# Optimization experiments

Hardware: AMD Instinct MI355X
Metric: run time of the kernel (lower is better)

The kernel has to match this reference:

```python
import jax, jax.numpy as jnp
import numpy as np

B, N, H = 32, 512, 128
LN_EPS = 1e-5

def _layernorm(x):
    # LayerNorm over last dim, no affine (elementwise_affine=False)
    mu = jnp.mean(x, axis=-1, keepdims=True)
    var = jnp.var(x, axis=-1, keepdims=True)
    return (x - mu) * jax.lax.rsqrt(var + LN_EPS)

def setup_inputs() -> dict:
    key = jax.random.key(0)
    k0, k1, k2, k3 = jax.random.split(key, 4)
    s = jax.random.normal(k0, (B, N, H), dtype=jnp.float32)
    ev = jax.random.normal(k1, (B, N, N, 3), dtype=jnp.float32)
    mask = (jax.random.uniform(k2, (B, N, N, 1)) > 0.5).astype(jnp.float32)
    W1 = jax.random.normal(k3, (H, H), dtype=jnp.float32) / np.sqrt(H)
    b1 = jnp.zeros((H,), dtype=jnp.float32)
    return {"s": s, "ev": ev, "mask": mask, "W1": W1, "b1": b1}

def reference(s, ev, mask, W1, b1):
    # lin1: Linear -> LayerNorm (no affine) -> SiLU
    h = jnp.einsum('bnh,kh->bnk', s, W1) + b1          # (B, N, H)
    h = jax.nn.silu(_layernorm(h))
    # Fused CFConv: v[b,i,c,d] = sum_j mask[b,i,j] * ev[b,i,j,c] * h[b,j,d]
    mev = ev * mask                                     # (B, N, N, 3)
    v = jnp.einsum('bijc,bjd->bicd', mev, h)            # (B, N, 3, H)
    return v
```

## Files before the change

kernel.cpp:

```cpp
#include <hip/hip_runtime.h>
#include <hip/hip_bf16.h>

#define B_ 32
#define N_ 512
#define H_ 128

typedef float f32x4 __attribute__((ext_vector_type(4)));
typedef short short8 __attribute__((ext_vector_type(8)));
typedef short short4v __attribute__((ext_vector_type(4)));

static __device__ __forceinline__ float bf2f(unsigned short u) {
  union { unsigned int ui; float f; } x;
  x.ui = ((unsigned int)u) << 16;
  return x.f;
}
static __device__ __forceinline__ unsigned short f2bf(float f) {
  __hip_bfloat16 h = __float2bfloat16(f);
  return *reinterpret_cast<unsigned short*>(&h);
}

__global__ __launch_bounds__(256, 2) void lin_ln_silu_kernel(
    const float* __restrict__ s, const float* __restrict__ W1,
    const float* __restrict__ b1, unsigned short* __restrict__ h_t) {
  __shared__ unsigned short sA[32 * 136];
  __shared__ unsigned short wB[128 * 136];
  __shared__ unsigned short ht_sh[128 * 40];
  __shared__ float buf[4][32][2];
  const int t = threadIdx.x;
  const int b = blockIdx.y;
  const int n0 = blockIdx.x * 32;
  const int w = t >> 6, l = t & 63;
  const int l15 = l & 15, quad = l >> 4;

#pragma unroll
  for (int r = 0; r < 16; ++r) {
    int q = t + 256 * r;
    int d = q >> 5, part = q & 31;
    float4 v = *reinterpret_cast<const float4*>(W1 + d * H_ + part * 4);
    short4v wv;
    wv.x = (short)f2bf(v.x); wv.y = (short)f2bf(v.y);
    wv.z = (short)f2bf(v.z); wv.w = (short)f2bf(v.w);
    *reinterpret_cast<short4v*>(&wB[d * 136 + part * 4]) = wv;
  }
#pragma unroll
  for (int r = 0; r < 4; ++r) {
    int q = t + 256 * r;
    int n = q >> 5, part = q & 31;
    float4 v = *reinterpret_cast<const float4*>(
        s + ((size_t)b * N_ + n0 + n) * H_ + part * 4);
    short4v sv;
    sv.x = (short)f2bf(v.x); sv.y = (short)f2bf(v.y);
    sv.z = (short)f2bf(v.z); sv.w = (short)f2bf(v.w);
    *reinterpret_cast<short4v*>(&sA[n * 136 + part * 4]) = sv;
  }
  __syncthreads();

  f32x4 acc[2][2];
#pragma unroll
  for (int mt = 0; mt < 2; ++mt)
#pragma unroll
    for (int ct = 0; ct < 2; ++ct)
#pragma unroll
      for (int e = 0; e < 4; ++e) acc[mt][ct][e] = 0.f;

#pragma unroll
  for (int ks = 0; ks < 4; ++ks) {
    short8 av[2], bv[2];
#pragma unroll
    for (int mt = 0; mt < 2; ++mt)
      av[mt] = *reinterpret_cast<const short8*>(
          &sA[(mt * 16 + l15) * 136 + ks * 32 + quad * 8]);
#pragma unroll
    for (int ct = 0; ct < 2; ++ct)
      bv[ct] = *reinterpret_cast<const short8*>(
          &wB[(w * 32 + ct * 16 + l15) * 136 + ks * 32 + quad * 8]);
#pragma unroll
    for (int mt = 0; mt < 2; ++mt)
#pragma unroll
      for (int ct = 0; ct < 2; ++ct)
        acc[mt][ct] = __builtin_amdgcn_mfma_f32_16x16x32_bf16(
            av[mt], bv[ct], acc[mt][ct], 0, 0, 0);
  }

  const float bb[2] = {b1[w * 32 + l15], b1[w * 32 + 16 + l15]};
#pragma unroll
  for (int mt = 0; mt < 2; ++mt)
#pragma unroll
    for (int ct = 0; ct < 2; ++ct)
#pragma unroll
      for (int e = 0; e < 4; ++e) acc[mt][ct][e] += bb[ct];

  float s1[2][4], s2[2][4];
#pragma unroll
  for (int mt = 0; mt < 2; ++mt)
#pragma unroll
    for (int r = 0; r < 4; ++r) {
      float x0 = acc[mt][0][r], x1 = acc[mt][1][r];
      s1[mt][r] = x0 + x1;
      s2[mt][r] = x0 * x0 + x1 * x1;
    }
#pragma unroll
  for (int off = 1; off <= 8; off <<= 1) {
#pragma unroll
    for (int mt = 0; mt < 2; ++mt)
#pragma unroll
      for (int r = 0; r < 4; ++r) {
        s1[mt][r] += __shfl_xor(s1[mt][r], off);
        s2[mt][r] += __shfl_xor(s2[mt][r], off);
      }
  }
  if (l15 == 0) {
#pragma unroll
    for (int mt = 0; mt < 2; ++mt)
#pragma unroll
      for (int r = 0; r < 4; ++r) {
        int row = mt * 16 + quad * 4 + r;
        buf[w][row][0] = s1[mt][r];
        buf[w][row][1] = s2[mt][r];
      }
  }
  __syncthreads();

#pragma unroll
  for (int mt = 0; mt < 2; ++mt)
#pragma unroll
    for (int r = 0; r < 4; ++r) {
      int row = mt * 16 + quad * 4 + r;
      float S1 = buf[0][row][0] + buf[1][row][0] + buf[2][row][0] +
                 buf[3][row][0];
      float S2 = buf[0][row][1] + buf[1][row][1] + buf[2][row][1] +
                 buf[3][row][1];
      float mean = S1 * (1.f / 128.f);
      float var = S2 * (1.f / 128.f) - mean * mean;
      float rs = rsqrtf(var + 1e-5f);
#pragma unroll
      for (int ct = 0; ct < 2; ++ct) {
        float x = (acc[mt][ct][r] - mean) * rs;
        float y = x / (1.f + __expf(-x));
        ht_sh[(w * 32 + ct * 16 + l15) * 40 + row] = f2bf(y);
      }
    }
  __syncthreads();

#pragma unroll
  for (int r = 0; r < 2; ++r) {
    int q = t + 256 * r;
    int d = q >> 2, part = q & 3;
    float4 v = *reinterpret_cast<const float4*>(&ht_sh[d * 40 + part * 8]);
    *reinterpret_cast<float4*>(
        h_t + ((size_t)b * 128 + d) * 512 + n0 + part * 8) = v;
  }
}

__global__ __launch_bounds__(256, 1) void cfconv_mfma_kernel(
    const float* __restrict__ ev, const float* __restrict__ mask,
    const unsigned short* __restrict__ h_t, float* __restrict__ out) {
  __shared__ unsigned short hL[128 * 512];
  const int t = threadIdx.x;
  const int b = blockIdx.y;
  const int i0 = blockIdx.x * 64;
  const int w = t >> 6, l = t & 63;
  const int l15 = l & 15, quad = l >> 4;
  const int ig = i0 + w * 16 + l15;

  {
    const unsigned short* hb = h_t + (size_t)b * 65536;
#pragma unroll 4
    for (int r2 = 0; r2 < 32; ++r2) {
      int row = w * 32 + r2;
      float4 v = *reinterpret_cast<const float4*>(hb + row * 512 + l * 8);
      *reinterpret_cast<float4*>(
          &hL[row * 512 + (l >> 3) * 64 + (((l & 7) ^ (row & 7)) * 8)]) = v;
    }
  }
  __syncthreads();

  f32x4 acc[3][8];
#pragma unroll
  for (int mt = 0; mt < 3; ++mt)
#pragma unroll
    for (int nt = 0; nt < 8; ++nt)
#pragma unroll
      for (int e = 0; e < 4; ++e) acc[mt][nt][e] = 0.f;

  const float* evrow =
      ev + ((size_t)(b * N_) + ig) * (N_ * 3) + quad * 24;
  const float* mrow = mask + ((size_t)(b * N_) + ig) * N_ + quad * 8;

  f32x4 evA[12], mkA[4], evB[12], mkB[4];
  short8 av[3][2];

#define ALOADO(DST, PTR, OFF)                                    \
  asm volatile("global_load_dwordx4 %0, %1, off offset:" OFF     \
               : "=v"(DST) : "v"(PTR))

#define ISSUE_SET(EVX, MKX, R)                                   \
  do {                                                           \
    const char* ep_ = (const char*)evrow + (R)*768;              \
    const char* mp_ = (const char*)mrow + (R)*256;               \
    ALOADO(EVX[0], ep_, "0");    ALOADO(EVX[1], ep_, "16");      \
    ALOADO(EVX[2], ep_, "32");   ALOADO(EVX[3], ep_, "48");      \
    ALOADO(EVX[4], ep_, "64");   ALOADO(EVX[5], ep_, "80");      \
    ALOADO(EVX[6], ep_, "384");  ALOADO(EVX[7], ep_, "400");     \
    ALOADO(EVX[8], ep_, "416");  ALOADO(EVX[9], ep_, "432");     \
    ALOADO(EVX[10], ep_, "448"); ALOADO(EVX[11], ep_, "464");    \
    ALOADO(MKX[0], mp_, "0");    ALOADO(MKX[1], mp_, "16");      \
    ALOADO(MKX[2], mp_, "128");  ALOADO(MKX[3], mp_, "144");     \
  } while (0)

#define VMW(n)                                       \
  do {                                               \
    asm volatile("s_waitcnt vmcnt(" #n ")");         \
    __builtin_amdgcn_sched_barrier(0);               \
  } while (0)

#define CONV(EVX, MKX)                                                  \
  do {                                                                  \
    _Pragma("unroll") for (int ks_ = 0; ks_ < 2; ++ks_) {               \
      float p_[8][3];                                                   \
      _Pragma("unroll") for (int e_ = 0; e_ < 8; ++e_) {                \
        float mv_ = MKX[ks_ * 2 + (e_ >> 2)][e_ & 3];                   \
        _Pragma("unroll") for (int c_ = 0; c_ < 3; ++c_) {              \
          int f_ = e_ * 3 + c_;                                         \
          p_[e_][c_] = EVX[ks_ * 6 + (f_ >> 2)][f_ & 3] * mv_;          \
        }                                                               \
      }                                                                 \
      _Pragma("unroll") for (int c_ = 0; c_ < 3; ++c_) {                \
        short8 a_;                                                      \
        _Pragma("unroll") for (int e_ = 0; e_ < 8; ++e_)                \
            a_[e_] = (short)f2bf(p_[e_][c_]);                           \
        av[c_][ks_] = a_;                                               \
      }                                                                 \
    }                                                                   \
  } while (0)

#define COMPUTE(J0)                                                     \
  do {                                                                  \
    _Pragma("unroll") for (int ks_ = 0; ks_ < 2; ++ks_) {               \
      _Pragma("unroll") for (int nt_ = 0; nt_ < 8; ++nt_) {             \
        int d_ = nt_ * 16 + l15;                                        \
        short8 bv_ = *reinterpret_cast<const short8*>(                  \
            &hL[d_ * 512 + (J0) +                                       \
                (((ks_ * 4 + quad) ^ (l15 & 7)) * 8)]);                 \
        _Pragma("unroll") for (int mt_ = 0; mt_ < 3; ++mt_)             \
            acc[mt_][nt_] = __builtin_amdgcn_mfma_f32_16x16x32_bf16(    \
                av[mt_][ks_], bv_, acc[mt_][nt_], 0, 0, 0);             \
      }                                                                 \
    }                                                                   \
  } while (0)

  ISSUE_SET(evA, mkA, 0);
  ISSUE_SET(evB, mkB, 1);

  VMW(16); CONV(evA, mkA); ISSUE_SET(evA, mkA, 2); COMPUTE(0);
  VMW(16); CONV(evB, mkB); ISSUE_SET(evB, mkB, 3); COMPUTE(64);
  VMW(16); CONV(evA, mkA); ISSUE_SET(evA, mkA, 4); COMPUTE(128);
  VMW(16); CONV(evB, mkB); ISSUE_SET(evB, mkB, 5); COMPUTE(192);
  VMW(16); CONV(evA, mkA); ISSUE_SET(evA, mkA, 6); COMPUTE(256);
  VMW(16); CONV(evB, mkB); ISSUE_SET(evB, mkB, 7); COMPUTE(320);
  VMW(16); CONV(evA, mkA); COMPUTE(384);
  VMW(0);  CONV(evB, mkB); COMPUTE(448);

#undef COMPUTE
#undef CONV
#undef VMW
#undef ISSUE_SET
#undef ALOADO

  __syncthreads();
  {
    float* zf = reinterpret_cast<float*>(hL) + w * 6144;
#pragma unroll
    for (int c = 0; c < 3; ++c)
#pragma unroll
      for (int nt = 0; nt < 8; ++nt)
#pragma unroll
        for (int r = 0; r < 4; ++r)
          zf[((quad * 4 + r) * 3 + c) * 128 + nt * 16 + l15] = acc[c][nt][r];
    asm volatile("s_waitcnt lgkmcnt(0)");
    __builtin_amdgcn_sched_barrier(0);
    float* ob = out + ((size_t)(b * N_) + i0 + w * 16) * 3 * 128;
#pragma unroll
    for (int k = 0; k < 24; ++k) {
      int flat = k * 256 + l * 4;
      f32x4 v = *reinterpret_cast<const f32x4*>(zf + flat);
      *reinterpret_cast<f32x4*>(ob + flat) = v;
    }
  }
}

extern "C" void kernel_launch(void* const* d_in, const int* in_sizes, int n_in,
                              void* d_out, int out_size, void* d_ws,
                              size_t ws_size, hipStream_t stream) {
  const float* s = (const float*)d_in[0];
  const float* ev = (const float*)d_in[1];
  const float* mask = (const float*)d_in[2];
  const float* W1 = (const float*)d_in[3];
  const float* b1 = (const float*)d_in[4];
  float* out = (float*)d_out;
  unsigned short* h_t = (unsigned short*)d_ws;

  lin_ln_silu_kernel<<<dim3(N_ / 32, B_), 256, 0, stream>>>(s, W1, b1, h_t);
  cfconv_mfma_kernel<<<dim3(N_ / 64, B_), 256, 0, stream>>>(ev, mask, h_t, out);
}
```

Measured before the change: 203.3 us.

## Split cfconv j-reduction across two wave groups with LDS reduction

```diff
diff --git a/kernel.cpp b/kernel.cpp
--- a/kernel.cpp
+++ b/kernel.cpp
@@ -152,7 +152,7 @@
   }
 }
 
-__global__ __launch_bounds__(256, 1) void cfconv_mfma_kernel(
+__global__ __launch_bounds__(512, 1) void cfconv_mfma_kernel(
     const float* __restrict__ ev, const float* __restrict__ mask,
     const unsigned short* __restrict__ h_t, float* __restrict__ out) {
   __shared__ unsigned short hL[128 * 512];
@@ -160,14 +160,15 @@
   const int b = blockIdx.y;
   const int i0 = blockIdx.x * 64;
   const int w = t >> 6, l = t & 63;
+  const int g = w & 3, jh = w >> 2;
   const int l15 = l & 15, quad = l >> 4;
-  const int ig = i0 + w * 16 + l15;
+  const int ig = i0 + g * 16 + l15;
 
   {
     const unsigned short* hb = h_t + (size_t)b * 65536;
 #pragma unroll 4
-    for (int r2 = 0; r2 < 32; ++r2) {
-      int row = w * 32 + r2;
+    for (int r2 = 0; r2 < 16; ++r2) {
+      int row = w * 16 + r2;
       float4 v = *reinterpret_cast<const float4*>(hb + row * 512 + l * 8);
       *reinterpret_cast<float4*>(
           &hL[row * 512 + (l >> 3) * 64 + (((l & 7) ^ (row & 7)) * 8)]) = v;
@@ -183,46 +184,48 @@
 #pragma unroll
       for (int e = 0; e < 4; ++e) acc[mt][nt][e] = 0.f;
 
-  const float* evrow =
-      ev + ((size_t)(b * N_) + ig) * (N_ * 3) + quad * 24;
-  const float* mrow = mask + ((size_t)(b * N_) + ig) * N_ + quad * 8;
-
-  f32x4 evA[12], mkA[4], evB[12], mkB[4];
+  const float* evrow = ev + ((size_t)(b * N_) + ig) * (N_ * 3) +
+                       jh * 768 + quad * 24;
+  const float* mrow = mask + ((size_t)(b * N_) + ig) * N_ +
+                      jh * 256 + quad * 8;
+  const int jbase = jh * 256;
+
+  f32x4 evv[12], mkv[4];
   short8 av[3][2];
 
 #define ALOADO(DST, PTR, OFF)                                    \
   asm volatile("global_load_dwordx4 %0, %1, off offset:" OFF     \
                : "=v"(DST) : "v"(PTR))
 
-#define ISSUE_SET(EVX, MKX, R)                                   \
+#define ISSUE_SET(R)                                             \
   do {                                                           \
     const char* ep_ = (const char*)evrow + (R)*768;              \
     const char* mp_ = (const char*)mrow + (R)*256;               \
-    ALOADO(EVX[0], ep_, "0");    ALOADO(EVX[1], ep_, "16");      \
-    ALOADO(EVX[2], ep_, "32");   ALOADO(EVX[3], ep_, "48");      \
-    ALOADO(EVX[4], ep_, "64");   ALOADO(EVX[5], ep_, "80");      \
-    ALOADO(EVX[6], ep_, "384");  ALOADO(EVX[7], ep_, "400");     \
-    ALOADO(EVX[8], ep_, "416");  ALOADO(EVX[9], ep_, "432");     \
-    ALOADO(EVX[10], ep_, "448"); ALOADO(EVX[11], ep_, "464");    \
-    ALOADO(MKX[0], mp_, "0");    ALOADO(MKX[1], mp_, "16");      \
-    ALOADO(MKX[2], mp_, "128");  ALOADO(MKX[3], mp_, "144");     \
+    ALOADO(evv[0], ep_, "0");    ALOADO(evv[1], ep_, "16");      \
+    ALOADO(evv[2], ep_, "32");   ALOADO(evv[3], ep_, "48");      \
+    ALOADO(evv[4], ep_, "64");   ALOADO(evv[5], ep_, "80");      \
+    ALOADO(evv[6], ep_, "384");  ALOADO(evv[7], ep_, "400");     \
+    ALOADO(evv[8], ep_, "416");  ALOADO(evv[9], ep_, "432");     \
+    ALOADO(evv[10], ep_, "448"); ALOADO(evv[11], ep_, "464");    \
+    ALOADO(mkv[0], mp_, "0");    ALOADO(mkv[1], mp_, "16");      \
+    ALOADO(mkv[2], mp_, "128");  ALOADO(mkv[3], mp_, "144");     \
   } while (0)
 
-#define VMW(n)                                       \
+#define VMW0()                                       \
   do {                                               \
-    asm volatile("s_waitcnt vmcnt(" #n ")");         \
+    asm volatile("s_waitcnt vmcnt(0)");              \
     __builtin_amdgcn_sched_barrier(0);               \
   } while (0)
 
-#define CONV(EVX, MKX)                                                  \
+#define CONV()                                                          \
   do {                                                                  \
     _Pragma("unroll") for (int ks_ = 0; ks_ < 2; ++ks_) {               \
       float p_[8][3];                                                   \
       _Pragma("unroll") for (int e_ = 0; e_ < 8; ++e_) {                \
-        float mv_ = MKX[ks_ * 2 + (e_ >> 2)][e_ & 3];                   \
+        float mv_ = mkv[ks_ * 2 + (e_ >> 2)][e_ & 3];                   \
         _Pragma("unroll") for (int c_ = 0; c_ < 3; ++c_) {              \
           int f_ = e_ * 3 + c_;                                         \
-          p_[e_][c_] = EVX[ks_ * 6 + (f_ >> 2)][f_ & 3] * mv_;          \
+          p_[e_][c_] = evv[ks_ * 6 + (f_ >> 2)][f_ & 3] * mv_;          \
         }                                                               \
       }                                                                 \
       _Pragma("unroll") for (int c_ = 0; c_ < 3; ++c_) {                \
@@ -249,27 +252,21 @@
     }                                                                   \
   } while (0)
 
-  ISSUE_SET(evA, mkA, 0);
-  ISSUE_SET(evB, mkB, 1);
-
-  VMW(16); CONV(evA, mkA); ISSUE_SET(evA, mkA, 2); COMPUTE(0);
-  VMW(16); CONV(evB, mkB); ISSUE_SET(evB, mkB, 3); COMPUTE(64);
-  VMW(16); CONV(evA, mkA); ISSUE_SET(evA, mkA, 4); COMPUTE(128);
-  VMW(16); CONV(evB, mkB); ISSUE_SET(evB, mkB, 5); COMPUTE(192);
-  VMW(16); CONV(evA, mkA); ISSUE_SET(evA, mkA, 6); COMPUTE(256);
-  VMW(16); CONV(evB, mkB); ISSUE_SET(evB, mkB, 7); COMPUTE(320);
-  VMW(16); CONV(evA, mkA); COMPUTE(384);
-  VMW(0);  CONV(evB, mkB); COMPUTE(448);
+  ISSUE_SET(0);
+  VMW0(); CONV(); ISSUE_SET(1); COMPUTE(jbase + 0);
+  VMW0(); CONV(); ISSUE_SET(2); COMPUTE(jbase + 64);
+  VMW0(); CONV(); ISSUE_SET(3); COMPUTE(jbase + 128);
+  VMW0(); CONV(); COMPUTE(jbase + 192);
 
 #undef COMPUTE
 #undef CONV
-#undef VMW
+#undef VMW0
 #undef ISSUE_SET
 #undef ALOADO
 
   __syncthreads();
-  {
-    float* zf = reinterpret_cast<float*>(hL) + w * 6144;
+  float* zf = reinterpret_cast<float*>(hL) + g * 6144;
+  if (jh == 1) {
 #pragma unroll
     for (int c = 0; c < 3; ++c)
 #pragma unroll
@@ -277,9 +274,21 @@
 #pragma unroll
         for (int r = 0; r < 4; ++r)
           zf[((quad * 4 + r) * 3 + c) * 128 + nt * 16 + l15] = acc[c][nt][r];
+  }
+  __syncthreads();
+  if (jh == 0) {
+#pragma unroll
+    for (int c = 0; c < 3; ++c)
+#pragma unroll
+      for (int nt = 0; nt < 8; ++nt)
+#pragma unroll
+        for (int r = 0; r < 4; ++r) {
+          int idx = ((quad * 4 + r) * 3 + c) * 128 + nt * 16 + l15;
+          zf[idx] += acc[c][nt][r];
+        }
     asm volatile("s_waitcnt lgkmcnt(0)");
     __builtin_amdgcn_sched_barrier(0);
-    float* ob = out + ((size_t)(b * N_) + i0 + w * 16) * 3 * 128;
+    float* ob = out + ((size_t)(b * N_) + i0 + g * 16) * 3 * 128;
 #pragma unroll
     for (int k = 0; k < 24; ++k) {
       int flat = k * 256 + l * 4;
@@ -301,5 +310,5 @@
   unsigned short* h_t = (unsigned short*)d_ws;
 
   lin_ln_silu_kernel<<<dim3(N_ / 32, B_), 256, 0, stream>>>(s, W1, b1, h_t);
-  cfconv_mfma_kernel<<<dim3(N_ / 64, B_), 256, 0, stream>>>(ev, mask, h_t, out);
-}
+  cfconv_mfma_kernel<<<dim3(N_ / 64, B_), 512, 0, stream>>>(ev, mask, h_t, out);
+}
```

Result: no change. 203.2 us (-0.1%).
